# Optimization experiments

Hardware: AMD Instinct MI355X
Metric: run time of the kernel (lower is better)

Reference implementation:

```python
import jax, jax.numpy as jnp
import numpy as np

BLOCK_LEN = 64

def setup_inputs() -> dict:
    key = jax.random.key(0)
    k1, k2, k3, k4 = jax.random.split(key, 4)
    b, s, h, p, n = 2, 4096, 16, 64, 128
    X = jax.random.normal(k1, (b, s, h, p), dtype=jnp.float32)
    # A scaled down so exp(cumsum) of the per-chunk decays stays finite in fp32
    A = jax.random.normal(k2, (b, s, h), dtype=jnp.float32) * 0.02
    B = jax.random.normal(k3, (b, s, h, n), dtype=jnp.float32)
    C = jax.random.normal(k4, (b, s, h, n), dtype=jnp.float32)
    return {"X": X, "A": A, "B": B, "C": C}

def reference(X, A, B, C):
    b, s, h, p = X.shape
    n = B.shape[-1]
    c = s // BLOCK_LEN
    # chunk the sequence: b (c l) ... -> b c l ...
    Xb = X.reshape(b, c, BLOCK_LEN, h, p)
    Bb = B.reshape(b, c, BLOCK_LEN, h, n)
    Ab = A.reshape(b, c, BLOCK_LEN, h).transpose(0, 3, 1, 2)  # b h c l
    A_cumsum = jnp.cumsum(Ab, axis=-1)                         # b h c l
    # decay from each position to the end of its chunk
    decay_states = jnp.exp(A_cumsum[..., -1:] - A_cumsum)      # b h c l
    # per-chunk states (end-of-chunk SSM state contribution)
    states = jnp.einsum('bclhn,bhcl,bclhp->bchpn', Bb, decay_states, Xb)
    init = jnp.zeros_like(states[:, :1])
    states = jnp.concatenate([init, states], axis=1)           # b (c+1) h p n
    # inter-chunk recurrence: only the LAST row of segsum_exp(pad(last_acum))
    # is consumed by new_states[:, -1]; row z=C equals exp(total - cumsum).
    last_acum = A_cumsum[..., -1]                              # b h c
    pad = jnp.pad(last_acum, ((0, 0), (0, 0), (1, 0)))         # b h (c+1)
    cp = jnp.cumsum(pad, axis=-1)
    decay_last = jnp.exp(cp[..., -1:] - cp)                    # b h (c+1)
    # final state after the whole sequence
    return jnp.einsum('bhc,bchpn->bhpn', decay_last, states)
```

## Files before the change

kernel.cpp:

```cpp
#include <hip/hip_runtime.h>
#include <hip/hip_bf16.h>

#define SLEN 4096
#define NH 16
#define PDIM 64
#define NDIM 128
#define NBH 32
#define KSPLIT 16
#define TT 64

typedef __attribute__((ext_vector_type(8))) short short8;
typedef __attribute__((ext_vector_type(4))) float f32x4;

#define BAR()                                                                  \
    {                                                                          \
        asm volatile("s_waitcnt lgkmcnt(0)" ::: "memory");                     \
        __builtin_amdgcn_sched_barrier(0);                                     \
        __builtin_amdgcn_s_barrier();                                          \
    }

__device__ __forceinline__ int swz(int r) { return ((r & 7) ^ ((r >> 2) & 7)) << 4; }

__device__ __forceinline__ unsigned short f2bfu(float x) {
    __hip_bfloat16 h = __float2bfloat16(x);
    return *reinterpret_cast<unsigned short*>(&h);
}
__device__ __forceinline__ unsigned pack2(float lo, float hi) {
    return (unsigned)f2bfu(lo) | ((unsigned)f2bfu(hi) << 16);
}

template <int KB, int NT>
__global__ __launch_bounds__(512, 4) void state_gemm_kernel(
    const float* __restrict__ X, const float* __restrict__ Bm,
    const float* __restrict__ A, float* __restrict__ partial) {
    int ks = blockIdx.x;
    int bh = blockIdx.y;
    int b = bh >> 4, h = bh & 15;
    int tid = threadIdx.x;
    int lane = tid & 63, wv_ = tid >> 6;
    int wp = wv_ & 1, wn = wv_ >> 1;
    int p0 = wp * 32, n0 = wn * 32;
    int m = lane & 15, kg = lane >> 4;
    int c = tid & 15, tp = tid >> 4;

    __shared__ __align__(16) char lds[2][24576];
    __shared__ float wlds[KB];

    const float* Xb = X + (size_t)b * (SLEN * NH * PDIM) + h * PDIM;
    const float* Bb = Bm + (size_t)b * (SLEN * NH * NDIM) + h * NDIM;
    const float* Ab = A + (size_t)b * (SLEN * NH) + h;
    int t0 = ks * KB;

    const float* xsrc = Xb + (size_t)(t0 + 2 * tp) * (NH * PDIM) + 4 * c;
    const float* bsrc = Bb + (size_t)(t0 + 2 * tp) * (NH * NDIM) + 4 * c;

    int wX[4];
#pragma unroll
    for (int i = 0; i < 4; ++i) {
        int r = 4 * c + i;
        wX[i] = (r * 128 + 4 * tp) ^ swz(r);
    }
    int rA[2][2], rB[2][2];
#pragma unroll
    for (int pi = 0; pi < 2; ++pi)
#pragma unroll
        for (int kk = 0; kk < 2; ++kk) {
            int r = p0 + pi * 16 + m;
            rA[pi][kk] = (r * 128 + kk * 64 + kg * 16) ^ swz(r);
        }
#pragma unroll
    for (int ni = 0; ni < 2; ++ni)
#pragma unroll
        for (int kk = 0; kk < 2; ++kk) {
            int rn = n0 + ni * 16 + m;
            rB[ni][kk] = 8192 + ((rn * 128 + kk * 64 + kg * 16) ^ swz(rn));
        }

    f32x4 acc[2][2];
#pragma unroll
    for (int i = 0; i < 2; ++i)
#pragma unroll
        for (int j = 0; j < 2; ++j) acc[i][j] = (f32x4){0.f, 0.f, 0.f, 0.f};

    f32x4 rx0[2], rx1[2], rb00[2], rb01[2], rb10[2], rb11[2];

#define LOADR(it, bk)                                                          \
    {                                                                          \
        const float* xp = xsrc + (size_t)(it) * (TT * NH * PDIM);              \
        const float* bp = bsrc + (size_t)(it) * (TT * NH * NDIM);              \
        rx0[bk] = *(const f32x4*)(xp);                                         \
        rx1[bk] = *(const f32x4*)(xp + NH * PDIM);                             \
        rb00[bk] = *(const f32x4*)(bp);                                        \
        rb01[bk] = *(const f32x4*)(bp + NH * NDIM);                            \
        rb10[bk] = *(const f32x4*)(bp + 64);                                   \
        rb11[bk] = *(const f32x4*)(bp + NH * NDIM + 64);                       \
    }

#define CVTW(buf, bk, it)                                                      \
    {                                                                          \
        float wv0 = wlds[(it) * TT + 2 * tp];                                  \
        float wv1 = wlds[(it) * TT + 2 * tp + 1];                              \
        char* dst = lds[buf];                                                  \
        _Pragma("unroll") for (int i = 0; i < 4; ++i) {                        \
            *(unsigned*)(dst + wX[i]) = pack2(rx0[bk][i] * wv0, rx1[bk][i] * wv1); \
            *(unsigned*)(dst + wX[i] + 8192) = pack2(rb00[bk][i], rb01[bk][i]);    \
            *(unsigned*)(dst + wX[i] + 16384) = pack2(rb10[bk][i], rb11[bk][i]);   \
        }                                                                      \
    }

#define COMPUTE(buf)                                                           \
    {                                                                          \
        const char* src = lds[buf];                                            \
        short8 af[2][2], bf[2][2];                                             \
        _Pragma("unroll") for (int pi = 0; pi < 2; ++pi)                       \
            _Pragma("unroll") for (int kk = 0; kk < 2; ++kk)                   \
                af[pi][kk] = *(const short8*)(src + rA[pi][kk]);               \
        _Pragma("unroll") for (int ni = 0; ni < 2; ++ni)                       \
            _Pragma("unroll") for (int kk = 0; kk < 2; ++kk)                   \
                bf[ni][kk] = *(const short8*)(src + rB[ni][kk]);               \
        _Pragma("unroll") for (int kk = 0; kk < 2; ++kk)                       \
            _Pragma("unroll") for (int pi = 0; pi < 2; ++pi)                   \
                _Pragma("unroll") for (int ni = 0; ni < 2; ++ni)               \
                    acc[pi][ni] = __builtin_amdgcn_mfma_f32_16x16x32_bf16(     \
                        af[pi][kk], bf[ni][kk], acc[pi][ni], 0, 0, 0);         \
    }

    LOADR(0, 0);
    if (NT > 1) LOADR(1, 1);

    {
        float* sc = (float*)(lds[1]);
        float ts = 0.f;
        for (int t = t0 + KB + tid; t < SLEN; t += 512) ts += Ab[(size_t)t * NH];
        constexpr int E = (KB + 511) / 512;
        float loc[E];
        float run = 0.f;
        int base = tid * E;
#pragma unroll
        for (int e = 0; e < E; ++e) {
            int idx = base + e;
            if (idx < KB) { run += Ab[(size_t)(t0 + idx) * NH]; loc[e] = run; }
        }
        float v = run;
#pragma unroll
        for (int off = 1; off < 64; off <<= 1) {
            float u = __shfl_up(v, off, 64);
            if (lane >= off) v += u;
        }
#pragma unroll
        for (int off = 32; off > 0; off >>= 1) ts += __shfl_xor(ts, off, 64);
        if (lane == 63) sc[wv_] = v;
        if (lane == 0) sc[8 + wv_] = ts;
        BAR();
        float woff = 0.f, tot = 0.f, stail = 0.f;
#pragma unroll
        for (int q = 0; q < 8; ++q) {
            float s_ = sc[q];
            tot += s_;
            if (q < wv_) woff += s_;
            stail += sc[8 + q];
        }
        float excl = woff + v - run;
        float basew = stail + tot;
#pragma unroll
        for (int e = 0; e < E; ++e) {
            int idx = base + e;
            if (idx < KB) wlds[idx] = expf(basew - (excl + loc[e]));
        }
        BAR();
    }

    CVTW(0, 0, 0);
    BAR();

#pragma unroll
    for (int it = 0; it < NT; ++it) {
        if (it + 2 < NT) LOADR(it + 2, it & 1);
        COMPUTE(it & 1);
        if (it + 1 < NT) CVTW((it + 1) & 1, (it + 1) & 1, it + 1);
        BAR();
    }
#undef LOADR
#undef CVTW
#undef COMPUTE

    float* outp = partial + ((size_t)ks * NBH + bh) * (PDIM * NDIM);
#pragma unroll
    for (int pi = 0; pi < 2; ++pi)
#pragma unroll
        for (int ni = 0; ni < 2; ++ni)
#pragma unroll
            for (int r = 0; r < 4; ++r) {
                int p = p0 + pi * 16 + kg * 4 + r;
                int n = n0 + ni * 16 + m;
                outp[p * NDIM + n] = acc[pi][ni][r];
            }
}

__global__ void reduce_kernel(const float* __restrict__ partial, float* __restrict__ out,
                              int ksplit) {
    int i = blockIdx.x * 256 + threadIdx.x;
    const f32x4* pp = (const f32x4*)partial;
    f32x4 s = (f32x4){0.f, 0.f, 0.f, 0.f};
    for (int ks = 0; ks < ksplit; ++ks) {
        f32x4 v = pp[(size_t)ks * (NBH * PDIM * NDIM / 4) + i];
        s.x += v.x; s.y += v.y; s.z += v.z; s.w += v.w;
    }
    ((f32x4*)out)[i] = s;
}

extern "C" void kernel_launch(void* const* d_in, const int* in_sizes, int n_in,
                              void* d_out, int out_size, void* d_ws, size_t ws_size,
                              hipStream_t stream) {
    const float* X = (const float*)d_in[0];
    const float* A = (const float*)d_in[1];
    const float* Bm = (const float*)d_in[2];
    float* out = (float*)d_out;

    float* partial = (float*)d_ws;
    size_t slice_bytes = (size_t)NBH * PDIM * NDIM * sizeof(float);

    if (ws_size < (size_t)KSPLIT * slice_bytes) {
        state_gemm_kernel<SLEN, SLEN / TT><<<dim3(1, NBH), 512, 0, stream>>>(X, Bm, A, out);
        return;
    }
    state_gemm_kernel<SLEN / KSPLIT, SLEN / KSPLIT / TT>
        <<<dim3(KSPLIT, NBH), 512, 0, stream>>>(X, Bm, A, partial);
    int nout4 = NBH * PDIM * NDIM / 4;
    reduce_kernel<<<nout4 / 256, 256, 0, stream>>>(partial, out, KSPLIT);
}
```

Measured before the change: 29.69 us.

## Split N dimension across two 256-thread blocks to double grid size

Each state GEMM block now covers half of the N dimension (64 columns) with 256 threads instead of all 128 columns with 512 threads. The grid gets an extra axis for the N-half, doubling the block count, and the per-block LDS staging shrinks from 24KB to 16KB per buffer. Each thread now loads four time rows per tile instead of two. The intent is more blocks for better CU occupancy and load balance. The cost is that X is loaded and converted twice (once per N-half), and the A-prefix scan is duplicated across both halves.

```diff
diff --git a/kernel.cpp b/kernel.cpp
--- a/kernel.cpp
+++ b/kernel.cpp
@@ -30,11 +30,12 @@
 }
 
 template <int KB, int NT>
-__global__ __launch_bounds__(512, 4) void state_gemm_kernel(
+__global__ __launch_bounds__(256, 4) void state_gemm_kernel(
     const float* __restrict__ X, const float* __restrict__ Bm,
     const float* __restrict__ A, float* __restrict__ partial) {
     int ks = blockIdx.x;
-    int bh = blockIdx.y;
+    int ns = blockIdx.y;
+    int bh = blockIdx.z;
     int b = bh >> 4, h = bh & 15;
     int tid = threadIdx.x;
     int lane = tid & 63, wv_ = tid >> 6;
@@ -43,11 +44,11 @@
     int m = lane & 15, kg = lane >> 4;
     int c = tid & 15, tp = tid >> 4;
 
-    __shared__ __align__(16) char lds[2][24576];
+    __shared__ __align__(16) char lds[2][16384];
     __shared__ float wlds[KB];
 
     const float* Xb = X + (size_t)b * (SLEN * NH * PDIM) + h * PDIM;
-    const float* Bb = Bm + (size_t)b * (SLEN * NH * NDIM) + h * NDIM;
+    const float* Bb = Bm + (size_t)b * (SLEN * NH * NDIM) + h * NDIM + ns * 64;
     const float* Ab = A + (size_t)b * (SLEN * NH) + h;
     int t0 = ks * KB;
 
@@ -82,29 +83,34 @@
 #pragma unroll
         for (int j = 0; j < 2; ++j) acc[i][j] = (f32x4){0.f, 0.f, 0.f, 0.f};
 
-    f32x4 rx0[2], rx1[2], rb00[2], rb01[2], rb10[2], rb11[2];
+    f32x4 xa[2], xb[2], xc[2], xd[2], ba[2], bb_[2], bc[2], bd[2];
 
 #define LOADR(it, bk)                                                          \
     {                                                                          \
         const float* xp = xsrc + (size_t)(it) * (TT * NH * PDIM);              \
         const float* bp = bsrc + (size_t)(it) * (TT * NH * NDIM);              \
-        rx0[bk] = *(const f32x4*)(xp);                                         \
-        rx1[bk] = *(const f32x4*)(xp + NH * PDIM);                             \
-        rb00[bk] = *(const f32x4*)(bp);                                        \
-        rb01[bk] = *(const f32x4*)(bp + NH * NDIM);                            \
-        rb10[bk] = *(const f32x4*)(bp + 64);                                   \
-        rb11[bk] = *(const f32x4*)(bp + NH * NDIM + 64);                       \
+        xa[bk] = *(const f32x4*)(xp);                                          \
+        xb[bk] = *(const f32x4*)(xp + NH * PDIM);                              \
+        xc[bk] = *(const f32x4*)(xp + 32 * NH * PDIM);                         \
+        xd[bk] = *(const f32x4*)(xp + 33 * NH * PDIM);                         \
+        ba[bk] = *(const f32x4*)(bp);                                          \
+        bb_[bk] = *(const f32x4*)(bp + NH * NDIM);                             \
+        bc[bk] = *(const f32x4*)(bp + 32 * NH * NDIM);                         \
+        bd[bk] = *(const f32x4*)(bp + 33 * NH * NDIM);                         \
     }
 
 #define CVTW(buf, bk, it)                                                      \
     {                                                                          \
-        float wv0 = wlds[(it) * TT + 2 * tp];                                  \
-        float wv1 = wlds[(it) * TT + 2 * tp + 1];                              \
+        float w0 = wlds[(it) * TT + 2 * tp];                                   \
+        float w1 = wlds[(it) * TT + 2 * tp + 1];                               \
+        float w2 = wlds[(it) * TT + 2 * tp + 32];                              \
+        float w3 = wlds[(it) * TT + 2 * tp + 33];                              \
         char* dst = lds[buf];                                                  \
         _Pragma("unroll") for (int i = 0; i < 4; ++i) {                        \
-            *(unsigned*)(dst + wX[i]) = pack2(rx0[bk][i] * wv0, rx1[bk][i] * wv1); \
-            *(unsigned*)(dst + wX[i] + 8192) = pack2(rb00[bk][i], rb01[bk][i]);    \
-            *(unsigned*)(dst + wX[i] + 16384) = pack2(rb10[bk][i], rb11[bk][i]);   \
+            *(unsigned*)(dst + wX[i]) = pack2(xa[bk][i] * w0, xb[bk][i] * w1); \
+            *(unsigned*)(dst + (wX[i] ^ 64)) = pack2(xc[bk][i] * w2, xd[bk][i] * w3); \
+            *(unsigned*)(dst + wX[i] + 8192) = pack2(ba[bk][i], bb_[bk][i]);   \
+            *(unsigned*)(dst + (wX[i] ^ 64) + 8192) = pack2(bc[bk][i], bd[bk][i]); \
         }                                                                      \
     }
 
@@ -131,8 +137,8 @@
     {
         float* sc = (float*)(lds[1]);
         float ts = 0.f;
-        for (int t = t0 + KB + tid; t < SLEN; t += 512) ts += Ab[(size_t)t * NH];
-        constexpr int E = (KB + 511) / 512;
+        for (int t = t0 + KB + tid; t < SLEN; t += 256) ts += Ab[(size_t)t * NH];
+        constexpr int E = (KB + 255) / 256;
         float loc[E];
         float run = 0.f;
         int base = tid * E;
@@ -150,15 +156,15 @@
 #pragma unroll
         for (int off = 32; off > 0; off >>= 1) ts += __shfl_xor(ts, off, 64);
         if (lane == 63) sc[wv_] = v;
-        if (lane == 0) sc[8 + wv_] = ts;
+        if (lane == 0) sc[4 + wv_] = ts;
         BAR();
         float woff = 0.f, tot = 0.f, stail = 0.f;
 #pragma unroll
-        for (int q = 0; q < 8; ++q) {
+        for (int q = 0; q < 4; ++q) {
             float s_ = sc[q];
             tot += s_;
             if (q < wv_) woff += s_;
-            stail += sc[8 + q];
+            stail += sc[4 + q];
         }
         float excl = woff + v - run;
         float basew = stail + tot;
@@ -184,7 +190,7 @@
 #undef CVTW
 #undef COMPUTE
 
-    float* outp = partial + ((size_t)ks * NBH + bh) * (PDIM * NDIM);
+    float* outp = partial + ((size_t)ks * NBH + bh) * (PDIM * NDIM) + ns * 64;
 #pragma unroll
     for (int pi = 0; pi < 2; ++pi)
 #pragma unroll
@@ -221,11 +227,11 @@
     size_t slice_bytes = (size_t)NBH * PDIM * NDIM * sizeof(float);
 
     if (ws_size < (size_t)KSPLIT * slice_bytes) {
-        state_gemm_kernel<SLEN, SLEN / TT><<<dim3(1, NBH), 512, 0, stream>>>(X, Bm, A, out);
+        state_gemm_kernel<SLEN, SLEN / TT><<<dim3(1, 2, NBH), 256, 0, stream>>>(X, Bm, A, out);
         return;
     }
     state_gemm_kernel<SLEN / KSPLIT, SLEN / KSPLIT / TT>
-        <<<dim3(KSPLIT, NBH), 512, 0, stream>>>(X, Bm, A, partial);
+        <<<dim3(KSPLIT, 2, NBH), 256, 0, stream>>>(X, Bm, A, partial);
     int nout4 = NBH * PDIM * NDIM / 4;
     reduce_kernel<<<nout4 / 256, 256, 0, stream>>>(partial, out, KSPLIT);
 }
```

After: 35.77 us. 1.2x slower.

## Double split-K, store bf16 partials, single-buffer LDS, and defer tail-decay scaling

Applied to the files above, without the earlier changes.

Raises the sequence split from 16 to 32 so more blocks run concurrently, and writes the per-split partial states in bf16 so partial traffic stays constant. The tail-decay sum is computed after the GEMM loop and applied as one output scale rather than folded into every weight. The LDS tile is single-buffered, with extra barriers per iteration, and A loads are hoisted. Storing bf16 partials lowers the precision of the reduction.

```diff
diff --git a/kernel.cpp b/kernel.cpp
--- a/kernel.cpp
+++ b/kernel.cpp
@@ -6,10 +6,11 @@
 #define PDIM 64
 #define NDIM 128
 #define NBH 32
-#define KSPLIT 16
+#define KSPLIT 32
 #define TT 64
 
 typedef __attribute__((ext_vector_type(8))) short short8;
+typedef __attribute__((ext_vector_type(8))) unsigned short ushort8;
 typedef __attribute__((ext_vector_type(4))) float f32x4;
 
 #define BAR()                                                                  \
@@ -29,10 +30,10 @@
     return (unsigned)f2bfu(lo) | ((unsigned)f2bfu(hi) << 16);
 }
 
-template <int KB, int NT>
+template <int KB, int NT, bool F32OUT>
 __global__ __launch_bounds__(512, 4) void state_gemm_kernel(
     const float* __restrict__ X, const float* __restrict__ Bm,
-    const float* __restrict__ A, float* __restrict__ partial) {
+    const float* __restrict__ A, void* __restrict__ partial) {
     int ks = blockIdx.x;
     int bh = blockIdx.y;
     int b = bh >> 4, h = bh & 15;
@@ -43,8 +44,10 @@
     int m = lane & 15, kg = lane >> 4;
     int c = tid & 15, tp = tid >> 4;
 
-    __shared__ __align__(16) char lds[2][24576];
+    __shared__ __align__(16) char lds[24576];
     __shared__ float wlds[KB];
+    __shared__ float sc[16];
+    __shared__ float sc2[8];
 
     const float* Xb = X + (size_t)b * (SLEN * NH * PDIM) + h * PDIM;
     const float* Bb = Bm + (size_t)b * (SLEN * NH * NDIM) + h * NDIM;
@@ -53,6 +56,17 @@
 
     const float* xsrc = Xb + (size_t)(t0 + 2 * tp) * (NH * PDIM) + 4 * c;
     const float* bsrc = Bb + (size_t)(t0 + 2 * tp) * (NH * NDIM) + 4 * c;
+
+    constexpr int E = (KB + 511) / 512;
+    float la[E];
+    {
+        int base = tid * E;
+#pragma unroll
+        for (int e = 0; e < E; ++e) {
+            int idx = base + e;
+            la[e] = (idx < KB) ? Ab[(size_t)(t0 + idx) * NH] : 0.f;
+        }
+    }
 
     int wX[4];
 #pragma unroll
@@ -96,11 +110,11 @@
         rb11[bk] = *(const f32x4*)(bp + NH * NDIM + 64);                       \
     }
 
-#define CVTW(buf, bk, it)                                                      \
+#define CVTW(bk, it)                                                           \
     {                                                                          \
         float wv0 = wlds[(it) * TT + 2 * tp];                                  \
         float wv1 = wlds[(it) * TT + 2 * tp + 1];                              \
-        char* dst = lds[buf];                                                  \
+        char* dst = lds;                                                       \
         _Pragma("unroll") for (int i = 0; i < 4; ++i) {                        \
             *(unsigned*)(dst + wX[i]) = pack2(rx0[bk][i] * wv0, rx1[bk][i] * wv1); \
             *(unsigned*)(dst + wX[i] + 8192) = pack2(rb00[bk][i], rb01[bk][i]);    \
@@ -108,9 +122,9 @@
         }                                                                      \
     }
 
-#define COMPUTE(buf)                                                           \
-    {                                                                          \
-        const char* src = lds[buf];                                            \
+#define COMPUTE()                                                              \
+    {                                                                          \
+        const char* src = lds;                                                 \
         short8 af[2][2], bf[2][2];                                             \
         _Pragma("unroll") for (int pi = 0; pi < 2; ++pi)                       \
             _Pragma("unroll") for (int kk = 0; kk < 2; ++kk)                   \
@@ -128,85 +142,118 @@
     LOADR(0, 0);
     if (NT > 1) LOADR(1, 1);
 
+    float tl[8];
+#pragma unroll
+    for (int i = 0; i < 8; ++i) {
+        int t = t0 + KB + tid + i * 512;
+        tl[i] = (t < SLEN) ? Ab[(size_t)t * NH] : 0.f;
+    }
+
     {
-        float* sc = (float*)(lds[1]);
-        float ts = 0.f;
-        for (int t = t0 + KB + tid; t < SLEN; t += 512) ts += Ab[(size_t)t * NH];
-        constexpr int E = (KB + 511) / 512;
         float loc[E];
         float run = 0.f;
-        int base = tid * E;
-#pragma unroll
-        for (int e = 0; e < E; ++e) {
-            int idx = base + e;
-            if (idx < KB) { run += Ab[(size_t)(t0 + idx) * NH]; loc[e] = run; }
-        }
+#pragma unroll
+        for (int e = 0; e < E; ++e) { run += la[e]; loc[e] = run; }
         float v = run;
 #pragma unroll
         for (int off = 1; off < 64; off <<= 1) {
             float u = __shfl_up(v, off, 64);
             if (lane >= off) v += u;
         }
-#pragma unroll
-        for (int off = 32; off > 0; off >>= 1) ts += __shfl_xor(ts, off, 64);
         if (lane == 63) sc[wv_] = v;
-        if (lane == 0) sc[8 + wv_] = ts;
         BAR();
-        float woff = 0.f, tot = 0.f, stail = 0.f;
+        float woff = 0.f, tot = 0.f;
 #pragma unroll
         for (int q = 0; q < 8; ++q) {
             float s_ = sc[q];
             tot += s_;
             if (q < wv_) woff += s_;
-            stail += sc[8 + q];
         }
         float excl = woff + v - run;
-        float basew = stail + tot;
+        int base = tid * E;
 #pragma unroll
         for (int e = 0; e < E; ++e) {
             int idx = base + e;
-            if (idx < KB) wlds[idx] = expf(basew - (excl + loc[e]));
+            if (idx < KB) wlds[idx] = expf(tot - (excl + loc[e]));
         }
         BAR();
     }
 
-    CVTW(0, 0, 0);
+    CVTW(0, 0);
     BAR();
 
-#pragma unroll
     for (int it = 0; it < NT; ++it) {
-        if (it + 2 < NT) LOADR(it + 2, it & 1);
-        COMPUTE(it & 1);
-        if (it + 1 < NT) CVTW((it + 1) & 1, (it + 1) & 1, it + 1);
-        BAR();
+        COMPUTE();
+        if (it + 1 < NT) {
+            BAR();
+            CVTW((it + 1) & 1, it + 1);
+            if (it + 2 < NT) LOADR(it + 2, (it + 2) & 1);
+            BAR();
+        }
     }
 #undef LOADR
 #undef CVTW
 #undef COMPUTE
 
-    float* outp = partial + ((size_t)ks * NBH + bh) * (PDIM * NDIM);
-#pragma unroll
-    for (int pi = 0; pi < 2; ++pi)
-#pragma unroll
-        for (int ni = 0; ni < 2; ++ni)
-#pragma unroll
-            for (int r = 0; r < 4; ++r) {
-                int p = p0 + pi * 16 + kg * 4 + r;
-                int n = n0 + ni * 16 + m;
-                outp[p * NDIM + n] = acc[pi][ni][r];
-            }
-}
-
-__global__ void reduce_kernel(const float* __restrict__ partial, float* __restrict__ out,
-                              int ksplit) {
+    float ts = 0.f;
+#pragma unroll
+    for (int i = 0; i < 8; ++i) ts += tl[i];
+#pragma unroll
+    for (int off = 32; off > 0; off >>= 1) ts += __shfl_xor(ts, off, 64);
+    if (lane == 0) sc2[wv_] = ts;
+    BAR();
+    float tsum = 0.f;
+#pragma unroll
+    for (int q = 0; q < 8; ++q) tsum += sc2[q];
+    float scale = expf(tsum);
+
+    if (F32OUT) {
+        float* outp = (float*)partial + ((size_t)ks * NBH + bh) * (PDIM * NDIM);
+#pragma unroll
+        for (int pi = 0; pi < 2; ++pi)
+#pragma unroll
+            for (int ni = 0; ni < 2; ++ni)
+#pragma unroll
+                for (int r = 0; r < 4; ++r) {
+                    int p = p0 + pi * 16 + kg * 4 + r;
+                    int n = n0 + ni * 16 + m;
+                    outp[p * NDIM + n] = acc[pi][ni][r] * scale;
+                }
+    } else {
+        __hip_bfloat16* outp =
+            (__hip_bfloat16*)partial + ((size_t)ks * NBH + bh) * (PDIM * NDIM);
+#pragma unroll
+        for (int pi = 0; pi < 2; ++pi)
+#pragma unroll
+            for (int ni = 0; ni < 2; ++ni)
+#pragma unroll
+                for (int r = 0; r < 4; ++r) {
+                    int p = p0 + pi * 16 + kg * 4 + r;
+                    int n = n0 + ni * 16 + m;
+                    outp[p * NDIM + n] = __float2bfloat16(acc[pi][ni][r] * scale);
+                }
+    }
+}
+
+__global__ void reduce_kernel(const __hip_bfloat16* __restrict__ partial,
+                              float* __restrict__ out, int ksplit) {
     int i = blockIdx.x * 256 + threadIdx.x;
-    const f32x4* pp = (const f32x4*)partial;
-    f32x4 s = (f32x4){0.f, 0.f, 0.f, 0.f};
+    float s[8];
+#pragma unroll
+    for (int j = 0; j < 8; ++j) s[j] = 0.f;
     for (int ks = 0; ks < ksplit; ++ks) {
-        f32x4 v = pp[(size_t)ks * (NBH * PDIM * NDIM / 4) + i];
-        s.x += v.x; s.y += v.y; s.z += v.z; s.w += v.w;
-    }
-    ((f32x4*)out)[i] = s;
+        ushort8 v = *(const ushort8*)((const unsigned short*)partial +
+                                      (size_t)ks * (NBH * PDIM * NDIM) + (size_t)i * 8);
+#pragma unroll
+        for (int j = 0; j < 8; ++j) {
+            unsigned u = ((unsigned)v[j]) << 16;
+            s[j] += *reinterpret_cast<float*>(&u);
+        }
+    }
+    f32x4 o0 = (f32x4){s[0], s[1], s[2], s[3]};
+    f32x4 o1 = (f32x4){s[4], s[5], s[6], s[7]};
+    *(f32x4*)(out + (size_t)i * 8) = o0;
+    *(f32x4*)(out + (size_t)i * 8 + 4) = o1;
 }
 
 extern "C" void kernel_launch(void* const* d_in, const int* in_sizes, int n_in,
@@ -217,15 +264,15 @@
     const float* Bm = (const float*)d_in[2];
     float* out = (float*)d_out;
 
-    float* partial = (float*)d_ws;
-    size_t slice_bytes = (size_t)NBH * PDIM * NDIM * sizeof(float);
-
-    if (ws_size < (size_t)KSPLIT * slice_bytes) {
-        state_gemm_kernel<SLEN, SLEN / TT><<<dim3(1, NBH), 512, 0, stream>>>(X, Bm, A, out);
+    size_t part_bytes = (size_t)KSPLIT * NBH * PDIM * NDIM * sizeof(__hip_bfloat16);
+
+    if (ws_size < part_bytes) {
+        state_gemm_kernel<SLEN, SLEN / TT, true>
+            <<<dim3(1, NBH), 512, 0, stream>>>(X, Bm, A, out);
         return;
     }
-    state_gemm_kernel<SLEN / KSPLIT, SLEN / KSPLIT / TT>
-        <<<dim3(KSPLIT, NBH), 512, 0, stream>>>(X, Bm, A, partial);
-    int nout4 = NBH * PDIM * NDIM / 4;
-    reduce_kernel<<<nout4 / 256, 256, 0, stream>>>(partial, out, KSPLIT);
-}
+    state_gemm_kernel<SLEN / KSPLIT, SLEN / KSPLIT / TT, false>
+        <<<dim3(KSPLIT, NBH), 512, 0, stream>>>(X, Bm, A, d_ws);
+    int ngrp = NBH * PDIM * NDIM / 8;
+    reduce_kernel<<<ngrp / 256, 256, 0, stream>>>((const __hip_bfloat16*)d_ws, out, KSPLIT);
+}
```

Measured after the change: 39.18 us. 31.9% more time.
